# Performance work log

Hardware: AMD Instinct MI355X
Metric: run time of the kernel (lower is better)

The kernel has to match this reference:

```python
import jax, jax.numpy as jnp
import numpy as np

HEAD = 12
EPS = float(np.finfo(np.float32).eps)  # torch RMSNorm default eps = finfo(dtype).eps


def _rmsnorm(v, g):
    # v: [B,H,T,dh], g: [dh]
    ms = jnp.mean(v * v, axis=-1, keepdims=True)
    return v * jax.lax.rsqrt(ms + EPS) * g


def setup_inputs() -> dict:
    key = jax.random.key(0)
    k1, k2, k3, k4, k5 = jax.random.split(key, 5)
    B, T, C = 2, 2048, 768
    x = jax.random.normal(k1, (B, T, C), dtype=jnp.float32)
    # nn.Linear(feats, feats, bias=False) weight: [out, in]
    W = jax.random.normal(k2, (C, C), dtype=jnp.float32) * (1.0 / np.sqrt(C))
    dh = C // HEAD
    g1 = jnp.ones((dh,), dtype=jnp.float32)
    g2 = jnp.ones((dh,), dtype=jnp.float32)
    g3 = jnp.ones((dh,), dtype=jnp.float32)
    return {"x": x, "W": W, "g1": g1, "g2": g2, "g3": g3}


def reference(x, W, g1, g2, g3):
    B, T, C = x.shape
    dh = C // HEAD
    sqrt_d = np.sqrt(dh).astype(np.float32)
    # qkv projection (shared weights): w = x @ W.T -> [B,H,T,dh]
    w = (x @ W.T).reshape(B, T, HEAD, dh).transpose(0, 2, 1, 3)
    q = _rmsnorm(w, g1)
    k = _rmsnorm(w, g2)
    v = _rmsnorm(w, g3)
    # full T x T score matrix (intentionally materialized, as in the module)
    att = jnp.einsum('bhif,bhjf->bhij', q, k) / sqrt_d
    a = jax.nn.softmax(att, axis=-1) + jax.nn.softmax(att, axis=-2)  # bisoftmax
    y = jnp.einsum('bhij,bhjf->bihf', a, v).reshape(B, T, C)
    # F.linear(y, W.t()) == y @ W
    return y @ W
```

## Files before the change

### kernel.cpp

```cpp
#include <hip/hip_runtime.h>

constexpr int T_SEQ = 2048;
constexpr int CDIM  = 768;
constexpr int HEADS = 12;
constexpr int DH    = 64;
constexpr int BATCH = 2;
constexpr int BH_TOT = BATCH * HEADS;
constexpr int NROWS  = BATCH * T_SEQ;
constexpr float RMS_EPS = 1.1920929e-07f;
constexpr float QSCALE = 0.18033688011112042f;


typedef __attribute__((ext_vector_type(8))) short bf16x8;
typedef __attribute__((ext_vector_type(4))) float f32x4;
typedef __attribute__((ext_vector_type(4))) unsigned int u32x4;

__device__ __forceinline__ unsigned short f2bf(float f) {
    union { float f; unsigned int u; } v; v.f = f;
    unsigned int u = v.u;
    unsigned int r = (u + 0x7fffu + ((u >> 16) & 1u)) >> 16;
    return (unsigned short)r;
}
__device__ __forceinline__ float b2f(unsigned short h) {
    union { unsigned int u; float f; } v; v.u = ((unsigned int)h) << 16;
    return v.f;
}
__device__ __forceinline__ unsigned int cvt_pk_bf16(float lo, float hi) {
    unsigned int r;
    asm("v_cvt_pk_bf16_f32 %0, %1, %2" : "=v"(r) : "v"(lo), "v"(hi));
    return r;
}
__device__ __forceinline__ float fast_exp2(float x) {
    float r;
    asm("v_exp_f32 %0, %1" : "=v"(r) : "v"(x));
    return r;
}
__device__ __forceinline__ void gld_lds16(const void* g, void* l) {
    __builtin_amdgcn_global_load_lds(
        (const __attribute__((address_space(1))) void*)g,
        (__attribute__((address_space(3))) void*)l, 16, 0, 0);
}
__device__ __forceinline__ void stageLin(const unsigned short* g, unsigned short* l, int tid) {
#pragma unroll
    for (int p = 0; p < 4; ++p) {
        int d = (p * 256 + tid) * 16;
        gld_lds16((const char*)g + d, (char*)l + d);
    }
}
__device__ __forceinline__ void stage8k(const unsigned short* g, unsigned short* l, int tid) {
#pragma unroll
    for (int p = 0; p < 2; ++p) {
        int d = (p * 256 + tid) * 16;
        gld_lds16((const char*)g + d, (char*)l + d);
    }
}

__global__ __launch_bounds__(256) void prep_kernel(
    const float* __restrict__ x, const float* __restrict__ W,
    unsigned short* __restrict__ xh,
    unsigned short* __restrict__ Wh, unsigned short* __restrict__ WTh)
{
    const size_t NC = (size_t)NROWS * CDIM;
    const size_t WSZ = (size_t)CDIM * CDIM;
    size_t stride = (size_t)gridDim.x * blockDim.x;
    for (size_t i = (size_t)blockIdx.x * blockDim.x + threadIdx.x; i < NC; i += stride)
        xh[i] = f2bf(x[i]);
    for (size_t i = (size_t)blockIdx.x * blockDim.x + threadIdx.x; i < WSZ; i += stride) {
        unsigned short h = f2bf(W[i]);
        Wh[i] = h;
        size_t k = i / CDIM, c = i % CDIM;
        WTh[c * CDIM + k] = h;
    }
}

__global__ __launch_bounds__(256) void gemm64_nt(
    const unsigned short* __restrict__ A, const unsigned short* __restrict__ B,
    float* __restrict__ C, int M, int N, int K, int ldc)
{
    __shared__ unsigned short sA[64 * 64], sB[64 * 64];
    const int tid = threadIdx.x;
    const int lane = tid & 63;
    const int wv = tid >> 6;
    const int wr = wv >> 1, wc = wv & 1;
    const int li = lane & 15, g = lane >> 4;

    const int nbx = N / 64;
    const int wgid = blockIdx.x;
    const int xcd = wgid & 7;
    const int idx = wgid >> 3;
    const int perx = (M / 64) / 8;
    const int my = xcd * perx + idx / nbx;
    const int nx = idx % nbx;
    const int M0 = my * 64, N0 = nx * 64;

    f32x4 acc[2][2];
#pragma unroll
    for (int i = 0; i < 2; ++i)
#pragma unroll
        for (int j = 0; j < 2; ++j) acc[i][j] = (f32x4)0.0f;

    for (int k0 = 0; k0 < K; k0 += 64) {
        __syncthreads();
#pragma unroll
        for (int p = 0; p < 2; ++p) {
            int dd = tid * 16 + p * 4096;
            int row = dd >> 7;
            int cb = (dd & 127) ^ ((row & 7) << 4);
            gld_lds16((const char*)A + ((size_t)(M0 + row) * K + k0) * 2 + cb, (char*)sA + dd);
            gld_lds16((const char*)B + ((size_t)(N0 + row) * K + k0) * 2 + cb, (char*)sB + dd);
        }
        __syncthreads();
#pragma unroll
        for (int ks = 0; ks < 2; ++ks) {
            const int ko = ks * 32 + g * 8;
            bf16x8 a[2], b[2];
#pragma unroll
            for (int mi = 0; mi < 2; ++mi) {
                int r = wr * 32 + mi * 16 + li;
                a[mi] = *(const bf16x8*)((char*)sA + ((r * 128 + ko * 2) ^ ((r & 7) << 4)));
            }
#pragma unroll
            for (int ni = 0; ni < 2; ++ni) {
                int r = wc * 32 + ni * 16 + li;
                b[ni] = *(const bf16x8*)((char*)sB + ((r * 128 + ko * 2) ^ ((r & 7) << 4)));
            }
#pragma unroll
            for (int mi = 0; mi < 2; ++mi)
#pragma unroll
                for (int ni = 0; ni < 2; ++ni)
                    acc[mi][ni] = __builtin_amdgcn_mfma_f32_16x16x32_bf16(a[mi], b[ni], acc[mi][ni], 0, 0, 0);
        }
    }
#pragma unroll
    for (int mi = 0; mi < 2; ++mi)
#pragma unroll
        for (int ni = 0; ni < 2; ++ni)
#pragma unroll
            for (int r = 0; r < 4; ++r) {
                int row = M0 + wr * 32 + mi * 16 + g * 4 + r;
                int col = N0 + wc * 32 + ni * 16 + li;
                C[(size_t)row * ldc + col] = acc[mi][ni][r];
            }
}

__global__ __launch_bounds__(256) void rmsqkv_kernel(
    const float* __restrict__ wbuf,
    const float* __restrict__ g1, const float* __restrict__ g2, const float* __restrict__ g3,
    unsigned short* __restrict__ qbf, unsigned short* __restrict__ kbf,
    unsigned short* __restrict__ vb)
{
    const int d = threadIdx.x & 63;
    const int wv = threadIdx.x >> 6;
    const int ridx = blockIdx.x * 4 + wv;
    const int bt = ridx / HEADS;
    const int h = ridx % HEADS;
    const int b = bt >> 11, t = bt & (T_SEQ - 1);

    float v = wbuf[(size_t)bt * CDIM + h * DH + d];
    float ss = v * v;
#pragma unroll
    for (int m = 32; m; m >>= 1) ss += __shfl_xor(ss, m);
    float r = rsqrtf(ss * (1.0f / 64.0f) + RMS_EPS);
    float wn = v * r;

    const int bh = b * HEADS + h;
    size_t fidx = (size_t)bh * (T_SEQ * DH)
                + (size_t)(t >> 7) * 8192
                + (size_t)((((t & 127) >> 4) * 2 + (d >> 5)) * 512
                           + ((d >> 3) & 3) * 128 + (t & 15) * 8 + (d & 7));
    qbf[fidx] = f2bf(wn * g1[d] * QSCALE);
    kbf[fidx] = f2bf(wn * g2[d]);
    vb[((size_t)bh * T_SEQ + t) * DH + d] = f2bf(wn * g3[d]);
}

__global__ __launch_bounds__(256) void vtrans_kernel(
    const unsigned short* __restrict__ vb, unsigned short* __restrict__ vTf)
{
    __shared__ unsigned short raw[128 * 72];
    const int bh = blockIdx.y, jt = blockIdx.x;
    const int tid = threadIdx.x;
    const unsigned short* src = &vb[((size_t)bh * T_SEQ + jt * 128) * DH];
#pragma unroll
    for (int p = 0; p < 4; ++p) {
        int i16 = p * 256 + tid;
        int r = i16 >> 3, c8 = i16 & 7;
        *(u32x4*)&raw[r * 72 + c8 * 8] = *(const u32x4*)&src[r * 64 + c8 * 8];
    }
    __syncthreads();
    unsigned short* dst = &vTf[(size_t)bh * (T_SEQ * DH) + (size_t)jt * 8192];
#pragma unroll
    for (int p = 0; p < 4; ++p) {
        int c = p * 256 + tid;
        int li = c & 15, g = (c >> 4) & 3, ni = (c >> 6) & 3, ks2 = c >> 8;
        int f = ni * 16 + li;
        int j0 = ks2 * 32 + g * 8;
        u32x4 out;
#pragma unroll
        for (int k = 0; k < 4; ++k) {
            unsigned int lo = raw[(j0 + 2 * k) * 72 + f];
            unsigned int hi = raw[(j0 + 2 * k + 1) * 72 + f];
            out[k] = lo | (hi << 16);
        }
        *(u32x4*)&dst[c * 8] = out;
    }
}

__global__ __launch_bounds__(256) void sums_kernel(
    const unsigned short* __restrict__ qbf, const unsigned short* __restrict__ kbf,
    float* __restrict__ rowsum, float* __restrict__ colsum)
{
    __shared__ unsigned short sQ[2][8192];
    const int tid = threadIdx.x;
    const int lane = tid & 63;
    const int w = tid >> 6;
    const int li = lane & 15;
    const int g = lane >> 4;

    const int wgid = blockIdx.x;
    const int xcd = wgid & 7;
    const int idx = wgid >> 3;
    const int bh = xcd * 3 + (idx >> 6);
    const int w2 = idx & 63;
    const int jx = w2 & 15;
    const int iy = w2 >> 4;
    const int J0 = jx * 128;

    const unsigned short* ktile = kbf + (size_t)bh * (T_SEQ * DH) + (size_t)jx * 8192;
    bf16x8 kf[2][2];
#pragma unroll
    for (int jb = 0; jb < 2; ++jb)
#pragma unroll
        for (int ks = 0; ks < 2; ++ks)
            kf[jb][ks] = *(const bf16x8*)&ktile[(size_t)((((w * 2 + jb) * 2 + ks) * 64 + lane) * 8)];

    const unsigned short* qbase = qbf + (size_t)bh * (T_SEQ * DH) + (size_t)(iy * 4) * 8192;
    stageLin(qbase, sQ[0], tid);
    __syncthreads();

    float csum[2][4];
#pragma unroll
    for (int jb = 0; jb < 2; ++jb)
#pragma unroll
        for (int r = 0; r < 4; ++r) csum[jb][r] = 0.0f;

    for (int it = 0; it < 4; ++it) {
        const int I0 = iy * 512 + it * 128;
        if (it + 1 < 4)
            stageLin(qbase + (size_t)(it + 1) * 8192, sQ[(it + 1) & 1], tid);
        const unsigned short* q = sQ[it & 1];

#pragma unroll
        for (int half = 0; half < 2; ++half) {
            f32x4 acc[2][4];
#pragma unroll
            for (int jb = 0; jb < 2; ++jb)
#pragma unroll
                for (int ib = 0; ib < 4; ++ib) acc[jb][ib] = (f32x4)0.0f;
#pragma unroll
            for (int ks = 0; ks < 2; ++ks) {
#pragma unroll
                for (int ib = 0; ib < 4; ++ib) {
                    bf16x8 qf = *(const bf16x8*)&q[(((half * 4 + ib) * 2 + ks) * 64 + lane) * 8];
#pragma unroll
                    for (int jb = 0; jb < 2; ++jb)
                        acc[jb][ib] = __builtin_amdgcn_mfma_f32_16x16x32_bf16(kf[jb][ks], qf, acc[jb][ib], 0, 0, 0);
                }
            }
#pragma unroll
            for (int ib = 0; ib < 4; ++ib) {
                float rp = 0.0f;
#pragma unroll
                for (int jb = 0; jb < 2; ++jb)
#pragma unroll
                    for (int r = 0; r < 4; ++r) {
                        float e = fast_exp2(acc[jb][ib][r]);
                        csum[jb][r] += e;
                        rp += e;
                    }
                rp += __shfl_xor(rp, 16);
                rp += __shfl_xor(rp, 32);
                if (g == 0)
                    atomicAdd(&rowsum[(size_t)bh * T_SEQ + I0 + half * 64 + ib * 16 + li], rp);
            }
        }
        __syncthreads();
    }
#pragma unroll
    for (int jb = 0; jb < 2; ++jb)
#pragma unroll
        for (int r = 0; r < 4; ++r) {
            float c = csum[jb][r];
            c += __shfl_xor(c, 1); c += __shfl_xor(c, 2);
            c += __shfl_xor(c, 4); c += __shfl_xor(c, 8);
            if (li == 0)
                atomicAdd(&colsum[(size_t)bh * T_SEQ + J0 + w * 32 + jb * 16 + g * 4 + r], c);
        }
}

__global__ __launch_bounds__(256) void inv_kernel(
    const float* __restrict__ rs, const float* __restrict__ cs,
    float* __restrict__ ri, float* __restrict__ ci_, int n)
{
    int i = blockIdx.x * 256 + threadIdx.x;
    if (i < n) { ri[i] = 1.0f / rs[i]; ci_[i] = 1.0f / cs[i]; }
}

__global__ __launch_bounds__(256) void fused_pv_kernel(
    const unsigned short* __restrict__ qbf, const unsigned short* __restrict__ kbf,
    const unsigned short* __restrict__ vTf,
    const float* __restrict__ rowinv, const float* __restrict__ colinv,
    unsigned short* __restrict__ yh)
{
    __shared__ unsigned short sK[4096];
    __shared__ unsigned short sV[4096];
    __shared__ unsigned short sP[4096];

    const int tid = threadIdx.x;
    const int lane = tid & 63;
    const int w = tid >> 6;
    const int li = lane & 15;
    const int g = lane >> 4;

    const int wgid = blockIdx.x;
    const int xcd = wgid & 7;
    const int idx = wgid >> 3;
    const int bh = xcd * 3 + (idx >> 5);
    const int it = idx & 31;
    const int I0 = it * 64;
    constexpr int NT = T_SEQ / 64;

    const int rbq = ((I0 & 127) >> 4) + w;
    const unsigned short* qtile = qbf + (size_t)bh * (T_SEQ * DH) + (size_t)(I0 >> 7) * 8192;
    bf16x8 qf[2];
#pragma unroll
    for (int ks = 0; ks < 2; ++ks)
        qf[ks] = *(const bf16x8*)&qtile[(size_t)(((rbq * 2 + ks) * 64 + lane) * 8)];
    const float rv = rowinv[bh * T_SEQ + I0 + w * 16 + li];

    char* const sPw = (char*)sP + w * 2048;

    f32x4 accy[4];
#pragma unroll
    for (int i = 0; i < 4; ++i) accy[i] = (f32x4)0.0f;

    const size_t bhbase = (size_t)bh * (T_SEQ * DH);
    const unsigned short* kt0 = kbf + bhbase;
    const unsigned short* vt0 = vTf + bhbase;

    stage8k(kt0, sK, tid);
    stage8k(vt0, sV, tid);
    __syncthreads();

    for (int jt = 0; jt < NT; ++jt) {
        f32x4 accs[4];
#pragma unroll
        for (int jb = 0; jb < 4; ++jb) accs[jb] = (f32x4)0.0f;
#pragma unroll
        for (int ks = 0; ks < 2; ++ks) {
#pragma unroll
            for (int jb = 0; jb < 4; ++jb) {
                bf16x8 kfr = *(const bf16x8*)&sK[((jb * 2 + ks) * 64 + lane) * 8];
                accs[jb] = __builtin_amdgcn_mfma_f32_16x16x32_bf16(kfr, qf[ks], accs[jb], 0, 0, 0);
            }
        }

#pragma unroll
        for (int jb = 0; jb < 4; ++jb) {
            f32x4 cv = *(const f32x4*)&colinv[(size_t)bh * T_SEQ + jt * 64 + jb * 16 + g * 4];
            float p0 = fast_exp2(accs[jb][0]) * (rv + cv[0]);
            float p1 = fast_exp2(accs[jb][1]) * (rv + cv[1]);
            float p2 = fast_exp2(accs[jb][2]) * (rv + cv[2]);
            float p3 = fast_exp2(accs[jb][3]) * (rv + cv[3]);
            uint2 pw;
            pw.x = cvt_pk_bf16(p0, p1);
            pw.y = cvt_pk_bf16(p2, p3);
            int off = ((jb >> 1) * 4 + (jb & 1) * 2 + (g >> 1)) * 256 + li * 16 + (g & 1) * 8;
            *(uint2*)(sPw + off) = pw;
        }

        __syncthreads();
        if (jt + 1 < NT)
            stage8k(kt0 + (size_t)(jt + 1) * 4096, sK, tid);

#pragma unroll
        for (int ks2 = 0; ks2 < 2; ++ks2) {
            bf16x8 pf = *(const bf16x8*)(sPw + ((ks2 * 4 + g) * 256 + li * 16));
#pragma unroll
            for (int ni = 0; ni < 4; ++ni) {
                bf16x8 vf = *(const bf16x8*)&sV[(ks2 * 256 + ni * 64 + lane) * 8];
                accy[ni] = __builtin_amdgcn_mfma_f32_16x16x32_bf16(pf, vf, accy[ni], 0, 0, 0);
            }
        }

        __syncthreads();
        if (jt + 1 < NT)
            stage8k(vt0 + (size_t)(jt + 1) * 4096, sV, tid);
    }

    const int b_ = bh / HEADS, h = bh % HEADS;
#pragma unroll
    for (int ni = 0; ni < 4; ++ni)
#pragma unroll
        for (int r = 0; r < 4; ++r) {
            int i = I0 + w * 16 + g * 4 + r;
            int col = h * DH + ni * 16 + li;
            yh[((size_t)b_ * T_SEQ + i) * CDIM + col] = f2bf(accy[ni][r]);
        }
}

extern "C" void kernel_launch(void* const* d_in, const int* in_sizes, int n_in,
                              void* d_out, int out_size, void* d_ws, size_t ws_size,
                              hipStream_t stream)
{
    const float* x  = (const float*)d_in[0];
    const float* W  = (const float*)d_in[1];
    const float* g1 = (const float*)d_in[2];
    const float* g2 = (const float*)d_in[3];
    const float* g3 = (const float*)d_in[4];
    float* out = (float*)d_out;

    char* p = (char*)d_ws;
    auto alloc = [&](size_t bytes) -> void* {
        void* r = (void*)p;
        p += (bytes + 255) & ~(size_t)255;
        return r;
    };
    const size_t NC  = (size_t)NROWS * CDIM;
    const size_t WSZ = (size_t)CDIM * CDIM;
    const size_t QSZ = (size_t)BH_TOT * T_SEQ * DH;

    unsigned short* xh   = (unsigned short*)alloc(NC * 2);
    unsigned short* Wh   = (unsigned short*)alloc(WSZ * 2);
    unsigned short* WTh  = (unsigned short*)alloc(WSZ * 2);
    float*          wbuf = (float*)alloc(NC * 4);
    unsigned short* qbf  = (unsigned short*)alloc(QSZ * 2);
    unsigned short* kbf  = (unsigned short*)alloc(QSZ * 2);
    unsigned short* vb   = (unsigned short*)alloc(QSZ * 2);
    unsigned short* vTf  = (unsigned short*)alloc(QSZ * 2);
    unsigned short* yh   = (unsigned short*)alloc(NC * 2);
    float* rowsum = (float*)alloc((size_t)BH_TOT * T_SEQ * 4);
    float* colsum = (float*)alloc((size_t)BH_TOT * T_SEQ * 4);
    float* rowinv = (float*)alloc((size_t)BH_TOT * T_SEQ * 4);
    float* colinv = (float*)alloc((size_t)BH_TOT * T_SEQ * 4);

    prep_kernel<<<2048, 256, 0, stream>>>(x, W, xh, Wh, WTh);
    gemm64_nt<<<(NROWS / 64) * (CDIM / 64), 256, 0, stream>>>(
        xh, Wh, wbuf, NROWS, CDIM, CDIM, CDIM);
    rmsqkv_kernel<<<(NROWS * HEADS) / 4, 256, 0, stream>>>(
        wbuf, g1, g2, g3, qbf, kbf, vb);
    vtrans_kernel<<<dim3(T_SEQ / 128, BH_TOT), 256, 0, stream>>>(vb, vTf);

    hipMemsetAsync(rowsum, 0, (size_t)BH_TOT * T_SEQ * 4, stream);
    hipMemsetAsync(colsum, 0, (size_t)BH_TOT * T_SEQ * 4, stream);
    sums_kernel<<<(T_SEQ / 128) * 4 * BH_TOT, 256, 0, stream>>>(
        qbf, kbf, rowsum, colsum);
    int n = BH_TOT * T_SEQ;
    inv_kernel<<<(n + 255) / 256, 256, 0, stream>>>(rowsum, colsum, rowinv, colinv, n);

    fused_pv_kernel<<<(T_SEQ / 64) * BH_TOT, 256, 0, stream>>>(
        qbf, kbf, vTf, rowinv, colinv, yh);

    gemm64_nt<<<(NROWS / 64) * (CDIM / 64), 256, 0, stream>>>(
        yh, WTh, out, NROWS, CDIM, CDIM, CDIM);
}
```

Measured before the change: 133.9 us.

## Fuse V transpose into RMSNorm kernel, shrink sums staging, add MFMA priority hints

The RMSNorm/QKV kernel now writes V straight into the transposed fragment layout that the PV kernel expects. This removes the separate vtrans kernel, its launch, and its intermediate buffer round-trip. The sums kernel now stages 64-row Q chunks (8 KB) double-buffered instead of 128-row chunks, which halves LDS use and may raise occupancy. s_setprio is raised around the MFMA loops in the sums and fused PV kernels. The scattered 2-byte V stores in the RMSNorm kernel may coalesce poorly.

```diff
diff --git a/kernel.cpp b/kernel.cpp
--- a/kernel.cpp
+++ b/kernel.cpp
@@ -39,13 +39,6 @@
     __builtin_amdgcn_global_load_lds(
         (const __attribute__((address_space(1))) void*)g,
         (__attribute__((address_space(3))) void*)l, 16, 0, 0);
-}
-__device__ __forceinline__ void stageLin(const unsigned short* g, unsigned short* l, int tid) {
-#pragma unroll
-    for (int p = 0; p < 4; ++p) {
-        int d = (p * 256 + tid) * 16;
-        gld_lds16((const char*)g + d, (char*)l + d);
-    }
 }
 __device__ __forceinline__ void stage8k(const unsigned short* g, unsigned short* l, int tid) {
 #pragma unroll
@@ -147,7 +140,7 @@
     const float* __restrict__ wbuf,
     const float* __restrict__ g1, const float* __restrict__ g2, const float* __restrict__ g3,
     unsigned short* __restrict__ qbf, unsigned short* __restrict__ kbf,
-    unsigned short* __restrict__ vb)
+    unsigned short* __restrict__ vTf)
 {
     const int d = threadIdx.x & 63;
     const int wv = threadIdx.x >> 6;
@@ -164,52 +157,24 @@
     float wn = v * r;
 
     const int bh = b * HEADS + h;
-    size_t fidx = (size_t)bh * (T_SEQ * DH)
-                + (size_t)(t >> 7) * 8192
+    const size_t base = (size_t)bh * (T_SEQ * DH) + (size_t)(t >> 7) * 8192;
+    size_t fidx = base
                 + (size_t)((((t & 127) >> 4) * 2 + (d >> 5)) * 512
                            + ((d >> 3) & 3) * 128 + (t & 15) * 8 + (d & 7));
     qbf[fidx] = f2bf(wn * g1[d] * QSCALE);
     kbf[fidx] = f2bf(wn * g2[d]);
-    vb[((size_t)bh * T_SEQ + t) * DH + d] = f2bf(wn * g3[d]);
-}
-
-__global__ __launch_bounds__(256) void vtrans_kernel(
-    const unsigned short* __restrict__ vb, unsigned short* __restrict__ vTf)
-{
-    __shared__ unsigned short raw[128 * 72];
-    const int bh = blockIdx.y, jt = blockIdx.x;
-    const int tid = threadIdx.x;
-    const unsigned short* src = &vb[((size_t)bh * T_SEQ + jt * 128) * DH];
-#pragma unroll
-    for (int p = 0; p < 4; ++p) {
-        int i16 = p * 256 + tid;
-        int r = i16 >> 3, c8 = i16 & 7;
-        *(u32x4*)&raw[r * 72 + c8 * 8] = *(const u32x4*)&src[r * 64 + c8 * 8];
-    }
-    __syncthreads();
-    unsigned short* dst = &vTf[(size_t)bh * (T_SEQ * DH) + (size_t)jt * 8192];
-#pragma unroll
-    for (int p = 0; p < 4; ++p) {
-        int c = p * 256 + tid;
-        int li = c & 15, g = (c >> 4) & 3, ni = (c >> 6) & 3, ks2 = c >> 8;
-        int f = ni * 16 + li;
-        int j0 = ks2 * 32 + g * 8;
-        u32x4 out;
-#pragma unroll
-        for (int k = 0; k < 4; ++k) {
-            unsigned int lo = raw[(j0 + 2 * k) * 72 + f];
-            unsigned int hi = raw[(j0 + 2 * k + 1) * 72 + f];
-            out[k] = lo | (hi << 16);
-        }
-        *(u32x4*)&dst[c * 8] = out;
-    }
+    const int jj = t & 127;
+    size_t vidx = base
+                + (size_t)(((jj >> 5) * 256 + (d >> 4) * 64 + ((jj >> 3) & 3) * 16 + (d & 15)) * 8
+                           + (jj & 7));
+    vTf[vidx] = f2bf(wn * g3[d]);
 }
 
 __global__ __launch_bounds__(256) void sums_kernel(
     const unsigned short* __restrict__ qbf, const unsigned short* __restrict__ kbf,
     float* __restrict__ rowsum, float* __restrict__ colsum)
 {
-    __shared__ unsigned short sQ[2][8192];
+    __shared__ unsigned short sQ[2][4096];
     const int tid = threadIdx.x;
     const int lane = tid & 63;
     const int w = tid >> 6;
@@ -233,8 +198,8 @@
         for (int ks = 0; ks < 2; ++ks)
             kf[jb][ks] = *(const bf16x8*)&ktile[(size_t)((((w * 2 + jb) * 2 + ks) * 64 + lane) * 8)];
 
-    const unsigned short* qbase = qbf + (size_t)bh * (T_SEQ * DH) + (size_t)(iy * 4) * 8192;
-    stageLin(qbase, sQ[0], tid);
+    const unsigned short* qbase = qbf + (size_t)bh * (T_SEQ * DH) + (size_t)(iy * 8) * 4096;
+    stage8k(qbase, sQ[0], tid);
     __syncthreads();
 
     float csum[2][4];
@@ -243,45 +208,44 @@
 #pragma unroll
         for (int r = 0; r < 4; ++r) csum[jb][r] = 0.0f;
 
-    for (int it = 0; it < 4; ++it) {
-        const int I0 = iy * 512 + it * 128;
-        if (it + 1 < 4)
-            stageLin(qbase + (size_t)(it + 1) * 8192, sQ[(it + 1) & 1], tid);
-        const unsigned short* q = sQ[it & 1];
-
-#pragma unroll
-        for (int half = 0; half < 2; ++half) {
-            f32x4 acc[2][4];
+    for (int st = 0; st < 8; ++st) {
+        const int I0 = iy * 512 + st * 64;
+        if (st + 1 < 8)
+            stage8k(qbase + (size_t)(st + 1) * 4096, sQ[(st + 1) & 1], tid);
+        const unsigned short* q = sQ[st & 1];
+
+        f32x4 acc[2][4];
+#pragma unroll
+        for (int jb = 0; jb < 2; ++jb)
+#pragma unroll
+            for (int ib = 0; ib < 4; ++ib) acc[jb][ib] = (f32x4)0.0f;
+        __builtin_amdgcn_s_setprio(1);
+#pragma unroll
+        for (int ks = 0; ks < 2; ++ks) {
+#pragma unroll
+            for (int ib = 0; ib < 4; ++ib) {
+                bf16x8 qf = *(const bf16x8*)&q[((ib * 2 + ks) * 64 + lane) * 8];
+#pragma unroll
+                for (int jb = 0; jb < 2; ++jb)
+                    acc[jb][ib] = __builtin_amdgcn_mfma_f32_16x16x32_bf16(kf[jb][ks], qf, acc[jb][ib], 0, 0, 0);
+            }
+        }
+        __builtin_amdgcn_s_setprio(0);
+#pragma unroll
+        for (int ib = 0; ib < 4; ++ib) {
+            float rp = 0.0f;
 #pragma unroll
             for (int jb = 0; jb < 2; ++jb)
 #pragma unroll
-                for (int ib = 0; ib < 4; ++ib) acc[jb][ib] = (f32x4)0.0f;
-#pragma unroll
-            for (int ks = 0; ks < 2; ++ks) {
-#pragma unroll
-                for (int ib = 0; ib < 4; ++ib) {
-                    bf16x8 qf = *(const bf16x8*)&q[(((half * 4 + ib) * 2 + ks) * 64 + lane) * 8];
-#pragma unroll
-                    for (int jb = 0; jb < 2; ++jb)
-                        acc[jb][ib] = __builtin_amdgcn_mfma_f32_16x16x32_bf16(kf[jb][ks], qf, acc[jb][ib], 0, 0, 0);
+                for (int r = 0; r < 4; ++r) {
+                    float e = fast_exp2(acc[jb][ib][r]);
+                    csum[jb][r] += e;
+                    rp += e;
                 }
-            }
-#pragma unroll
-            for (int ib = 0; ib < 4; ++ib) {
-                float rp = 0.0f;
-#pragma unroll
-                for (int jb = 0; jb < 2; ++jb)
-#pragma unroll
-                    for (int r = 0; r < 4; ++r) {
-                        float e = fast_exp2(acc[jb][ib][r]);
-                        csum[jb][r] += e;
-                        rp += e;
-                    }
-                rp += __shfl_xor(rp, 16);
-                rp += __shfl_xor(rp, 32);
-                if (g == 0)
-                    atomicAdd(&rowsum[(size_t)bh * T_SEQ + I0 + half * 64 + ib * 16 + li], rp);
-            }
+            rp += __shfl_xor(rp, 16);
+            rp += __shfl_xor(rp, 32);
+            if (g == 0)
+                atomicAdd(&rowsum[(size_t)bh * T_SEQ + I0 + ib * 16 + li], rp);
         }
         __syncthreads();
     }
@@ -355,6 +319,7 @@
         f32x4 accs[4];
 #pragma unroll
         for (int jb = 0; jb < 4; ++jb) accs[jb] = (f32x4)0.0f;
+        __builtin_amdgcn_s_setprio(1);
 #pragma unroll
         for (int ks = 0; ks < 2; ++ks) {
 #pragma unroll
@@ -363,6 +328,7 @@
                 accs[jb] = __builtin_amdgcn_mfma_f32_16x16x32_bf16(kfr, qf[ks], accs[jb], 0, 0, 0);
             }
         }
+        __builtin_amdgcn_s_setprio(0);
 
 #pragma unroll
         for (int jb = 0; jb < 4; ++jb) {
@@ -382,6 +348,7 @@
         if (jt + 1 < NT)
             stage8k(kt0 + (size_t)(jt + 1) * 4096, sK, tid);
 
+        __builtin_amdgcn_s_setprio(1);
 #pragma unroll
         for (int ks2 = 0; ks2 < 2; ++ks2) {
             bf16x8 pf = *(const bf16x8*)(sPw + ((ks2 * 4 + g) * 256 + li * 16));
@@ -391,6 +358,7 @@
                 accy[ni] = __builtin_amdgcn_mfma_f32_16x16x32_bf16(pf, vf, accy[ni], 0, 0, 0);
             }
         }
+        __builtin_amdgcn_s_setprio(0);
 
         __syncthreads();
         if (jt + 1 < NT)
@@ -435,7 +403,6 @@
     float*          wbuf = (float*)alloc(NC * 4);
     unsigned short* qbf  = (unsigned short*)alloc(QSZ * 2);
     unsigned short* kbf  = (unsigned short*)alloc(QSZ * 2);
-    unsigned short* vb   = (unsigned short*)alloc(QSZ * 2);
     unsigned short* vTf  = (unsigned short*)alloc(QSZ * 2);
     unsigned short* yh   = (unsigned short*)alloc(NC * 2);
     float* rowsum = (float*)alloc((size_t)BH_TOT * T_SEQ * 4);
@@ -447,8 +414,7 @@
     gemm64_nt<<<(NROWS / 64) * (CDIM / 64), 256, 0, stream>>>(
         xh, Wh, wbuf, NROWS, CDIM, CDIM, CDIM);
     rmsqkv_kernel<<<(NROWS * HEADS) / 4, 256, 0, stream>>>(
-        wbuf, g1, g2, g3, qbf, kbf, vb);
-    vtrans_kernel<<<dim3(T_SEQ / 128, BH_TOT), 256, 0, stream>>>(vb, vTf);
+        wbuf, g1, g2, g3, qbf, kbf, vTf);
 
     hipMemsetAsync(rowsum, 0, (size_t)BH_TOT * T_SEQ * 4, stream);
     hipMemsetAsync(colsum, 0, (size_t)BH_TOT * T_SEQ * 4, stream);
```

After: 139.1 us. 1.04x slower.
